# Optimization experiments

Hardware: AMD Instinct MI355X
Metric: run time of the kernel (lower is better)

## Reference

```python
import jax, jax.numpy as jnp
import numpy as np

B, C_IN, C_H, C_OUT, H, W = 2, 512, 512, 512, 14, 14


def setup_inputs() -> dict:
    key = jax.random.key(0)
    ks = jax.random.split(key, 6)
    s_in = 1.0 / np.sqrt(C_IN + C_H)   # torch Linear init bound for in_linear
    s_out = 1.0 / np.sqrt(C_H)          # torch Linear init bound for out_linear
    return {
        "input": jax.random.normal(ks[0], (B, C_IN, H, W), jnp.float32),
        # in_linear weight (C_H, C_IN + C_H) split into x-part and h-part
        "Wx": jax.random.uniform(ks[1], (C_H, C_IN), jnp.float32, -s_in, s_in),
        "Wh": jax.random.uniform(ks[2], (C_H, C_H), jnp.float32, -s_in, s_in),
        "b_in": jax.random.uniform(ks[3], (C_H,), jnp.float32, -s_in, s_in),
        "Wo": jax.random.uniform(ks[4], (C_OUT, C_H), jnp.float32, -s_out, s_out),
        "b_out": jax.random.uniform(ks[5], (C_OUT,), jnp.float32, -s_out, s_out),
    }


def reference(input, Wx, Wh, b_in, Wo, b_out):
    Bn, _, Hn, Wn = input.shape
    hid = Wh.shape[0]
    # four scan directions = four flips of the input (outputs are summed in
    # flipped coordinates, exactly as the original torch code does -- no unflip)
    x_modes = jnp.stack([
        input,
        jnp.flip(input, 3),
        jnp.flip(input, 2),
        jnp.flip(jnp.flip(input, 2), 3),
    ])  # (4, B, C_IN, H, W)
    rows = jnp.arange(Hn)
    cols = jnp.arange(Wn)

    def run_mode(x):
        # x-contribution of in_linear, shared by every (i,j) in the window
        a = jnp.einsum('hc,bcxy->bhxy', Wx, x) + b_in[None, :, None, None]

        def step(h, p):
            px, py = p // Wn, p % Wn
            # h_vivj over the full grid; cells outside the causal window hold
            # h == 0 and are masked out of the sum below (softmax is per-pixel
            # over channels, so no cross-pixel contamination)
            z = jax.nn.relu(a[:, :, px, py][:, :, None, None]
                            + jnp.einsum('ch,bhxy->bcxy', Wh, h))
            sm = jax.nn.softmax(z, axis=1)  # Softmax(dim=1): over channels
            mask = (rows[:, None] <= px) & (cols[None, :] <= py)  # (H, W)
            h_vi = jnp.sum(z * sm * mask, axis=(2, 3))  # (B, hid)
            h = h.at[:, :, px, py].set(h_vi)
            y_vi = h_vi @ Wo.T + b_out
            return h, y_vi

        h0 = jnp.zeros((Bn, hid, Hn, Wn), input.dtype)
        _, ys = jax.lax.scan(step, h0, jnp.arange(Hn * Wn))
        # ys: (H*W, B, C_OUT) -> (B, C_OUT, H, W) in raster order
        return ys.reshape(Hn, Wn, Bn, -1).transpose(2, 3, 0, 1)

    y = jax.vmap(run_mode)(x_modes).sum(axis=0)  # sum over the 4 directions
    return jax.nn.softmax(y, axis=1)
```

## Files before the change

kernel.cpp:

```cpp
#include <hip/hip_runtime.h>
#include <hip/hip_bf16.h>

#define BB 2
#define CC 512
#define HH 14
#define WW 14
#define PP 196
#define NSEQ 8
#define NSLICE 8
#define NWORK (14 * NSLICE)
#define FW 16
#define NZERO (3 * PP * FW)
#define ALL8 0x0101010101010101ull


__global__ __launch_bounds__(256) void prep(
    const float* __restrict__ Wx, const float* __restrict__ X,
    const float* __restrict__ b_in, const float* __restrict__ Wh,
    float* __restrict__ A, float* __restrict__ WhT,
    unsigned* __restrict__ cnts ) {
    __shared__ float Ws[32][33], Xs[32][33];
    int bid = blockIdx.x;
    int t = threadIdx.x;
    if (bid < 224) {
        int z = bid / 112, rem = bid % 112;
        int c0 = (rem % 16) * 32, p0 = (rem / 16) * 32;
        int tx = t % 32, ty = t / 32;
        int pl = (t % 16) * 2, cl = (t / 16) * 2;
        float acc[2][2] = {{0.f,0.f},{0.f,0.f}};
        for (int k0 = 0; k0 < CC; k0 += 32) {
            #pragma unroll
            for (int r = 0; r < 4; ++r)
                Ws[ty + 8*r][tx] = Wx[(size_t)(c0 + ty + 8*r) * CC + k0 + tx];
            #pragma unroll
            for (int r = 0; r < 4; ++r) {
                int p = p0 + tx, k = k0 + ty + 8*r;
                Xs[ty + 8*r][tx] = (p < PP) ? X[((size_t)z * CC + k) * PP + p] : 0.f;
            }
            __syncthreads();
            #pragma unroll
            for (int k = 0; k < 32; ++k) {
                float w0 = Ws[cl][k], w1 = Ws[cl+1][k];
                float x0 = Xs[k][pl], x1 = Xs[k][pl+1];
                acc[0][0] += w0*x0; acc[0][1] += w0*x1;
                acc[1][0] += w1*x0; acc[1][1] += w1*x1;
            }
            __syncthreads();
        }
        #pragma unroll
        for (int i = 0; i < 2; ++i)
            #pragma unroll
            for (int j = 0; j < 2; ++j) {
                int c = c0 + cl + i, p = p0 + pl + j;
                if (p < PP) A[((size_t)z * PP + p) * CC + c] = acc[i][j] + b_in[c];
            }
    } else if (bid < 480) {
        int tid = bid - 224;
        int c0 = (tid % 16) * 32, k0 = (tid / 16) * 32;
        int tx = t % 32, ty = t / 32;
        #pragma unroll
        for (int r = 0; r < 4; ++r)
            Ws[ty + 8*r][tx] = Wh[(size_t)(c0 + ty + 8*r) * CC + k0 + tx];
        __syncthreads();
        #pragma unroll
        for (int r = 0; r < 4; ++r)
            WhT[(size_t)(k0 + ty + 8*r) * CC + c0 + tx] = Ws[tx][ty + 8*r];
    } else {
        for (int i = t; i < NZERO; i += 256) cnts[i] = 0u;
    }
}

__device__ __forceinline__ unsigned long long flag8_ld(const unsigned char* f) {
    return __hip_atomic_load((const unsigned long long*)f, __ATOMIC_RELAXED,
                             __HIP_MEMORY_SCOPE_AGENT);
}
__device__ __forceinline__ void flag_st(unsigned char* f) {
    __hip_atomic_store(f, (unsigned char)1, __ATOMIC_RELAXED,
                       __HIP_MEMORY_SCOPE_AGENT);
}
__device__ __forceinline__ float ldf_agent(const float* p) {
    return __hip_atomic_load(p, __ATOMIC_RELAXED, __HIP_MEMORY_SCOPE_AGENT);
}
__device__ __forceinline__ void store_wt(float* p, float v) {
    __hip_atomic_store(p, v, __ATOMIC_RELAXED, __HIP_MEMORY_SCOPE_AGENT);
}

__device__ __forceinline__ void pix(const float4 E0, const float4 E1,
                                    const float* ar, const float* er, float* hacc) {
    float ee[8] = {E0.x,E0.y,E0.z,E0.w,E1.x,E1.y,E1.z,E1.w};
    float ds = 0.f, tl[8];
    #pragma unroll
    for (int j = 0; j < 8; ++j) {
        float sv = ar[j] + __logf(ee[j]);
        float pv = er[j] * ee[j];
        ds += fmaxf(pv, 1.0f);
        tl[j] = fmaxf(sv, 0.0f) * pv;
    }
    #pragma unroll
    for (int off = 32; off; off >>= 1) ds += __shfl_xor(ds, off, 64);
    float rd = 1.0f / ds;
    #pragma unroll
    for (int j = 0; j < 8; ++j) hacc[j] += tl[j] * rd;
}

__device__ __forceinline__ void proc_row(const float* __restrict__ rowp, int n,
                                         const float* ar, const float* er, float* hacc) {
    float4 cur[4][2];
    int y = 0, curn = (n < 4) ? n : 4;
    #pragma unroll
    for (int i = 0; i < 4; ++i) if (i < curn) {
        cur[i][0] = *(const float4*)(rowp + (size_t)i * CC);
        cur[i][1] = *(const float4*)(rowp + (size_t)i * CC + 256);
    }
    while (true) {
        int yn = y + curn;
        int rem = n - yn;
        int nextn = (rem < 4) ? rem : 4;
        float4 nxt[4][2];
        #pragma unroll
        for (int i = 0; i < 4; ++i) if (i < nextn) {
            nxt[i][0] = *(const float4*)(rowp + (size_t)(yn + i) * CC);
            nxt[i][1] = *(const float4*)(rowp + (size_t)(yn + i) * CC + 256);
        }
        #pragma unroll
        for (int i = 0; i < 4; ++i) if (i < curn)
            pix(cur[i][0], cur[i][1], ar, er, hacc);
        if (nextn <= 0) break;
        #pragma unroll
        for (int i = 0; i < 4; ++i) if (i < nextn) {
            cur[i][0] = nxt[i][0]; cur[i][1] = nxt[i][1];
        }
        curn = nextn; y = yn;
    }
}

__global__ __launch_bounds__(512, 2) void rnn_dataflow(
    const float* __restrict__ A, const float* __restrict__ WhT,
    float* __restrict__ E, float* __restrict__ h_bulk,
    float* __restrict__ h_t, float* __restrict__ TLN,
    float* __restrict__ TLW, float* __restrict__ dsAcc,
    unsigned char* __restrict__ uflag, unsigned char* __restrict__ hflag) {
    __shared__ __align__(16) float hT8[CC * 8];
    __shared__ __align__(16) float up[8 * 576];
    __shared__ unsigned mbox;
    __shared__ unsigned pf;
    int bid = blockIdx.x;
    int t = threadIdx.x;
    int lane = t & 63, wv = t >> 6;

    if (bid < NWORK) {
        int px = bid >> 3, w = bid & 7;
        int ch = w * 64 + lane;
        int m = wv >> 1, b = wv & 1;
        float wreg2[64];
        #pragma unroll
        for (int kk = 0; kk < 64; ++kk)
            wreg2[kk] = WhT[(size_t)(wv * 64 + kk) * CC + ch];
        __builtin_amdgcn_s_setprio(1);

        float hb[8];
        float tnr[8], dsNr[8];
        bool hb_ok = false;
        bool n_ok  = false;

        for (int py = 0; py < WW; ++py) {
            int cell = px * WW + py;
            int cellN = cell - WW, cellW = cell - 1;

            float aSr = 0.f, aWr = 0.f;
            if (px < HH - 1) {
                int fi = (m & 2) ? (HH - 2 - px) : (px + 1);
                int fj = (m & 1) ? (WW - 1 - py) : py;
                aSr = A[((size_t)b * PP + fi * WW + fj) * CC + ch];
            }
            if (py < WW - 1) {
                int fi = (m & 2) ? (HH - 1 - px) : px;
                int fj = (m & 1) ? (WW - 2 - py) : (py + 1);
                aWr = A[((size_t)b * PP + fi * WW + fj) * CC + ch];
            }

            if (!hb_ok) {
                if (wv == 0 && lane == 0)
                    while (flag8_ld(hflag + (size_t)cell * 64) != ALL8)
                        __builtin_amdgcn_s_sleep(1);
                __syncthreads();
                asm volatile("" ::: "memory");
                #pragma unroll
                for (int s = 0; s < 8; ++s)
                    hb[s] = h_bulk[((size_t)cell * NSEQ + s) * CC + t];
            }

            if (wv == 0) {
                while (true) {
                    unsigned ok = 1u;
                    if (lane == 0)      { if (py > 0) ok = (flag8_ld(uflag + (size_t)cellW * 64) == ALL8); }
                    else if (lane == 1) { if (px > 0 && !n_ok) ok = (flag8_ld(uflag + (size_t)cellN * 64) == ALL8); }
                    if (__ballot(ok != 0u) == ~0ull) break;
                    __builtin_amdgcn_s_sleep(1);
                }
            }
            __syncthreads();
            asm volatile("" ::: "memory");

            if (px > 0) {
                if (!n_ok) {
                    #pragma unroll
                    for (int i = 0; i < 8; ++i)
                        dsNr[i] = ldf_agent(&dsAcc[(size_t)cell * 16 + i]);
                    #pragma unroll
                    for (int s = 0; s < 8; ++s)
                        tnr[s] = ldf_agent(&TLN[((size_t)cell * NSEQ + s) * CC + t]);
                }
                #pragma unroll
                for (int s = 0; s < 8; ++s)
                    hb[s] += tnr[s] * __builtin_amdgcn_rcpf(dsNr[s]);
            }
            if (py > 0) {
                float dsw[8], tw[8];
                #pragma unroll
                for (int i = 0; i < 8; ++i)
                    dsw[i] = ldf_agent(&dsAcc[(size_t)cell * 16 + 8 + i]);
                #pragma unroll
                for (int s = 0; s < 8; ++s)
                    tw[s] = ldf_agent(&TLW[((size_t)cell * NSEQ + s) * CC + t]);
                #pragma unroll
                for (int s = 0; s < 8; ++s)
                    hb[s] += tw[s] * __builtin_amdgcn_rcpf(dsw[s]);
            }
            if (wv == w) {
                #pragma unroll
                for (int s = 0; s < 8; ++s)
                    h_t[((size_t)cell * NSEQ + s) * CC + t] = hb[s];
            }
            *(float4*)&hT8[t * 8]     = make_float4(hb[0], hb[1], hb[2], hb[3]);
            *(float4*)&hT8[t * 8 + 4] = make_float4(hb[4], hb[5], hb[6], hb[7]);
            if (cell == PP - 1) break;

            float acc[8] = {0.f,0.f,0.f,0.f,0.f,0.f,0.f,0.f};
            const float* hp = hT8 + (wv << 9);
            #pragma unroll
            for (int kk = 0; kk < 64; ++kk) {
                float4 h0 = *(const float4*)(hp + kk * 8);
                float4 h1 = *(const float4*)(hp + kk * 8 + 4);
                float wvv = wreg2[kk];
                acc[0] += wvv * h0.x; acc[1] += wvv * h0.y;
                acc[2] += wvv * h0.z; acc[3] += wvv * h0.w;
                acc[4] += wvv * h1.x; acc[5] += wvv * h1.y;
                acc[6] += wvv * h1.z; acc[7] += wvv * h1.w;
            }
            #pragma unroll
            for (int s = 0; s < 8; ++s)
                up[wv * 576 + lane * 9 + s] = acc[s];
            __syncthreads();

            {
                float U = up[lane * 9 + wv];
                #pragma unroll
                for (int w2 = 1; w2 < 8; ++w2) U += up[w2 * 576 + lane * 9 + wv];
                float Ev = __expf(U);
                store_wt(&E[((size_t)wv * PP + cell) * CC + ch], Ev);
                float pdS = 0.f, pdW = 0.f;
                if (px < HH - 1) {
                    float pv = __expf(aSr) * Ev;
                    store_wt(&TLN[((size_t)(cell + WW) * NSEQ + wv) * CC + ch],
                             fmaxf(aSr + U, 0.f) * pv);
                    pdS = fmaxf(pv, 1.f);
                }
                if (py < WW - 1) {
                    float pv = __expf(aWr) * Ev;
                    store_wt(&TLW[((size_t)(cell + 1) * NSEQ + wv) * CC + ch],
                             fmaxf(aWr + U, 0.f) * pv);
                    pdW = fmaxf(pv, 1.f);
                }
                #pragma unroll
                for (int off = 32; off; off >>= 1) {
                    pdS += __shfl_xor(pdS, off, 64);
                    pdW += __shfl_xor(pdW, off, 64);
                }
                if (lane == 0) {
                    if (px < HH - 1)
                        unsafeAtomicAdd(&dsAcc[(size_t)(cell + WW) * 16 + wv], pdS);
                    if (py < WW - 1)
                        unsafeAtomicAdd(&dsAcc[(size_t)(cell + 1) * 16 + 8 + wv], pdW);
                }
            }

            if (t == 0) {
                unsigned v = 0u;
                if (py + 1 < WW) {
                    if (flag8_ld(hflag + (size_t)(cell + 1) * 64) == ALL8) v |= 1u;
                    if (px > 0 &&
                        flag8_ld(uflag + (size_t)(cellN + 1) * 64) == ALL8) v |= 2u;
                }
                pf = v;
            }

            __syncthreads();
            if (t == 0) flag_st(uflag + (size_t)cell * 64 + w);

            hb_ok = false; n_ok = false;
            if (py + 1 < WW) {
                unsigned v = pf;
                if (v & 1u) {
                    #pragma unroll
                    for (int s = 0; s < 8; ++s)
                        hb[s] = h_bulk[((size_t)(cell + 1) * NSEQ + s) * CC + t];
                    hb_ok = true;
                }
                if (v & 2u) {
                    #pragma unroll
                    for (int i = 0; i < 8; ++i)
                        dsNr[i] = ldf_agent(&dsAcc[(size_t)(cell + 1) * 16 + i]);
                    #pragma unroll
                    for (int s = 0; s < 8; ++s)
                        tnr[s] = ldf_agent(&TLN[((size_t)(cell + 1) * NSEQ + s) * CC + t]);
                    n_ok = true;
                }
            }
        }
    } else {
        int cell = bid - NWORK;
        int px = cell / WW, py = cell % WW;
        int s = wv, m = s >> 1, b = s & 1;
        int fi = (m & 2) ? (HH-1-px) : px;
        int fj = (m & 1) ? (WW-1-py) : py;
        int cb = lane * 4;

        if (t == 0) mbox = 0u;
        __syncthreads();

        const float* acur = A + ((size_t)b * PP + fi * WW + fj) * CC;
        float4 a0 = *(const float4*)(acur + cb);
        float4 a1 = *(const float4*)(acur + cb + 256);
        float ar[8] = {a0.x,a0.y,a0.z,a0.w,a1.x,a1.y,a1.z,a1.w};
        float er[8];
        #pragma unroll
        for (int j = 0; j < 8; ++j) er[j] = __expf(ar[j]);
        float hacc[8] = {0.f,0.f,0.f,0.f,0.f,0.f,0.f,0.f};

        {
            float ds = 0.f, tl[8];
            #pragma unroll
            for (int j = 0; j < 8; ++j) {
                float pv = er[j];
                ds += fmaxf(pv, 1.0f);
                tl[j] = fmaxf(ar[j], 0.0f) * pv;
            }
            #pragma unroll
            for (int off = 32; off; off >>= 1) ds += __shfl_xor(ds, off, 64);
            float rd = 1.0f / ds;
            #pragma unroll
            for (int j = 0; j < 8; ++j) hacc[j] += tl[j] * rd;
        }

        const float* Eb = E + (size_t)s * PP * CC;
        int sx = lane >> 1, sph = lane & 1;
        int gate = -1;
        if (sx <= px) {
            int L = (sx <= px-2) ? py : ((sx == px-1) ? py-1 : py-2);
            if (L >= 0) {
                if (L <= 2) { if (sph == 0) gate = sx * WW + L; }
                else gate = sx * WW + (sph ? L : (L - 3));
            }
        }
        unsigned pend = (unsigned)__ballot(gate >= 0);

        if (wv == 0) {
            unsigned done = 0u;
            while (pend) {
                bool rdy = true;
                if (gate >= 0 && ((pend >> lane) & 1u))
                    rdy = (flag8_ld(uflag + (size_t)gate * 64) == ALL8);
                unsigned newly = pend & (unsigned)__ballot(rdy);
                if (!newly) { __builtin_amdgcn_s_sleep(2); continue; }
                done |= newly;
                __hip_atomic_store(&mbox, done, __ATOMIC_RELAXED,
                                   __HIP_MEMORY_SCOPE_WORKGROUP);
                asm volatile("" ::: "memory");
                unsigned go = newly;
                while (go) {
                    int sl = __ffs(go) - 1; go &= go - 1;
                    int xx = sl >> 1;
                    int L = (xx <= px-2) ? py : ((xx == px-1) ? py-1 : py-2);
                    int yy0 = 0, yy1 = L;
                    if (L > 2) { if (sl & 1) yy0 = L - 2; else yy1 = L - 3; }
                    proc_row(Eb + (size_t)(xx * WW + yy0) * CC + cb,
                             yy1 - yy0 + 1, ar, er, hacc);
                }
                pend &= ~newly;
            }
        } else {
            while (pend) {
                unsigned d = __hip_atomic_load(&mbox, __ATOMIC_RELAXED,
                                               __HIP_MEMORY_SCOPE_WORKGROUP);
                unsigned newly = d & pend;
                if (!newly) { __builtin_amdgcn_s_sleep(2); continue; }
                asm volatile("" ::: "memory");
                unsigned go = newly;
                while (go) {
                    int sl = __ffs(go) - 1; go &= go - 1;
                    int xx = sl >> 1;
                    int L = (xx <= px-2) ? py : ((xx == px-1) ? py-1 : py-2);
                    int yy0 = 0, yy1 = L;
                    if (L > 2) { if (sl & 1) yy0 = L - 2; else yy1 = L - 3; }
                    proc_row(Eb + (size_t)(xx * WW + yy0) * CC + cb,
                             yy1 - yy0 + 1, ar, er, hacc);
                }
                pend &= ~newly;
            }
        }

        float* hp = h_bulk + ((size_t)cell * NSEQ + s) * CC;
        #pragma unroll
        for (int j = 0; j < 4; ++j) {
            store_wt(hp + cb + j,       hacc[j]);
            store_wt(hp + cb + 256 + j, hacc[4 + j]);
        }
        __builtin_amdgcn_s_waitcnt(0);
        asm volatile("" ::: "memory");
        if (lane == 0) flag_st(hflag + (size_t)cell * 64 + s);
    }
}

__global__ __launch_bounds__(256) void gemm_y(
    const float* __restrict__ Wo, const float* __restrict__ h_t,
    const float* __restrict__ b_out, float* __restrict__ Y) {
    __shared__ float Ws[32][33], Hs[32][33];
    int b  = blockIdx.z;
    int c0 = blockIdx.x * 32, p0 = blockIdx.y * 32;
    int t  = threadIdx.x;
    int tx = t % 32, ty = t / 32;
    int pl = (t % 16) * 2, cl = (t / 16) * 2;
    float acc[2][2] = {{0.f,0.f},{0.f,0.f}};
    for (int k0 = 0; k0 < CC; k0 += 32) {
        #pragma unroll
        for (int r = 0; r < 4; ++r)
            Ws[ty + 8*r][tx] = Wo[(size_t)(c0 + ty + 8*r) * CC + k0 + tx];
        #pragma unroll
        for (int r = 0; r < 4; ++r) {
            int p = p0 + ty + 8*r;
            float v = 0.f;
            if (p < PP) {
                size_t base = (size_t)p * NSEQ * CC + k0 + tx;
                v = h_t[base + (size_t)(0 + b) * CC]
                  + h_t[base + (size_t)(2 + b) * CC]
                  + h_t[base + (size_t)(4 + b) * CC]
                  + h_t[base + (size_t)(6 + b) * CC];
            }
            Hs[tx][ty + 8*r] = v;
        }
        __syncthreads();
        #pragma unroll
        for (int k = 0; k < 32; ++k) {
            float w0 = Ws[cl][k], w1 = Ws[cl+1][k];
            float h0 = Hs[k][pl], h1 = Hs[k][pl+1];
            acc[0][0] += w0*h0; acc[0][1] += w0*h1;
            acc[1][0] += w1*h0; acc[1][1] += w1*h1;
        }
        __syncthreads();
    }
    #pragma unroll
    for (int i = 0; i < 2; ++i)
        #pragma unroll
        for (int j = 0; j < 2; ++j) {
            int cc = c0 + cl + i, p = p0 + pl + j;
            if (p < PP) Y[((size_t)b * PP + p) * CC + cc] = acc[i][j] + 4.0f * b_out[cc];
        }
}

__global__ __launch_bounds__(256) void softmax_out(
    const float* __restrict__ Y, float* __restrict__ out) {
    int wave = threadIdx.x >> 6, lane = threadIdx.x & 63;
    int idx = blockIdx.x * 4 + wave;
    if (idx >= BB * PP) return;
    int b = idx / PP, p = idx % PP;
    const float* y = Y + ((size_t)b * PP + p) * CC;
    float v[8];
    float mx = -3.4e38f;
    #pragma unroll
    for (int j = 0; j < 8; ++j) { v[j] = y[lane + 64*j]; mx = fmaxf(mx, v[j]); }
    #pragma unroll
    for (int off = 32; off; off >>= 1) mx = fmaxf(mx, __shfl_xor(mx, off, 64));
    float sum = 0.f;
    #pragma unroll
    for (int j = 0; j < 8; ++j) { v[j] = expf(v[j] - mx); sum += v[j]; }
    #pragma unroll
    for (int off = 32; off; off >>= 1) sum += __shfl_xor(sum, off, 64);
    float r = 1.0f / sum;
    #pragma unroll
    for (int j = 0; j < 8; ++j)
        out[((size_t)b * CC + lane + 64*j) * PP + p] = v[j] * r;
}

extern "C" void kernel_launch(void* const* d_in, const int* in_sizes, int n_in,
                              void* d_out, int out_size, void* d_ws, size_t ws_size,
                              hipStream_t stream) {
    const float* X     = (const float*)d_in[0];
    const float* Wx    = (const float*)d_in[1];
    const float* Wh    = (const float*)d_in[2];
    const float* b_in  = (const float*)d_in[3];
    const float* Wo    = (const float*)d_in[4];
    const float* b_out = (const float*)d_in[5];
    float* out = (float*)d_out;

    float* ws     = (float*)d_ws;
    float* WhT    = ws;
    float* A      = WhT    + 262144;
    float* E      = A      + 200704;
    float* h_bulk = E      + 802816;
    float* h_t    = h_bulk + 802816;
    float* TLN    = h_t    + 802816;
    float* TLW    = TLN    + 802816;
    float* Y      = TLW    + 802816;
    unsigned char* uflag = (unsigned char*)(Y + 200704);
    unsigned char* hflag = uflag + PP * 64;
    float* dsAcc = (float*)(hflag + PP * 64);

    hipLaunchKernelGGL(prep, dim3(481), dim3(256), 0, stream,
                       Wx, X, b_in, Wh, A, WhT, (unsigned*)uflag);
    hipLaunchKernelGGL(rnn_dataflow, dim3(NWORK + PP), dim3(512), 0, stream,
                       A, WhT, E, h_bulk, h_t, TLN, TLW, dsAcc, uflag, hflag);
    hipLaunchKernelGGL(gemm_y, dim3(16, 7, 2), dim3(256), 0, stream, Wo, h_t, b_out, Y);
    hipLaunchKernelGGL(softmax_out, dim3(98), dim3(256), 0, stream, Y, out);
}
```

Baseline: 349.9 us.

## Fuse output projection and softmax into dataflow kernel via per-cell flags

Measured after the change: 319.4 us. 1.1x faster.

```diff
diff --git a/kernel.cpp b/kernel.cpp
--- a/kernel.cpp
+++ b/kernel.cpp
@@ -17,7 +17,8 @@
 __global__ __launch_bounds__(256) void prep(
     const float* __restrict__ Wx, const float* __restrict__ X,
     const float* __restrict__ b_in, const float* __restrict__ Wh,
-    float* __restrict__ A, float* __restrict__ WhT,
+    const float* __restrict__ Wo,
+    float* __restrict__ A, float* __restrict__ WhT, float* __restrict__ WoT,
     unsigned* __restrict__ cnts ) {
     __shared__ float Ws[32][33], Xs[32][33];
     int bid = blockIdx.x;
@@ -54,17 +55,20 @@
                 int c = c0 + cl + i, p = p0 + pl + j;
                 if (p < PP) A[((size_t)z * PP + p) * CC + c] = acc[i][j] + b_in[c];
             }
-    } else if (bid < 480) {
+    } else if (bid < 736) {
         int tid = bid - 224;
+        const float* src = (tid < 256) ? Wh : Wo;
+        float* dst = (tid < 256) ? WhT : WoT;
+        tid &= 255;
         int c0 = (tid % 16) * 32, k0 = (tid / 16) * 32;
         int tx = t % 32, ty = t / 32;
         #pragma unroll
         for (int r = 0; r < 4; ++r)
-            Ws[ty + 8*r][tx] = Wh[(size_t)(c0 + ty + 8*r) * CC + k0 + tx];
+            Ws[ty + 8*r][tx] = src[(size_t)(c0 + ty + 8*r) * CC + k0 + tx];
         __syncthreads();
         #pragma unroll
         for (int r = 0; r < 4; ++r)
-            WhT[(size_t)(k0 + ty + 8*r) * CC + c0 + tx] = Ws[tx][ty + 8*r];
+            dst[(size_t)(k0 + ty + 8*r) * CC + c0 + tx] = Ws[tx][ty + 8*r];
     } else {
         for (int i = t; i < NZERO; i += 256) cnts[i] = 0u;
     }
@@ -139,7 +143,9 @@
     float* __restrict__ E, float* __restrict__ h_bulk,
     float* __restrict__ h_t, float* __restrict__ TLN,
     float* __restrict__ TLW, float* __restrict__ dsAcc,
-    unsigned char* __restrict__ uflag, unsigned char* __restrict__ hflag) {
+    unsigned char* __restrict__ uflag, unsigned char* __restrict__ hflag,
+    const float* __restrict__ WoT, const float* __restrict__ b_out,
+    float* __restrict__ out) {
     __shared__ __align__(16) float hT8[CC * 8];
     __shared__ __align__(16) float up[8 * 576];
     __shared__ unsigned mbox;
@@ -230,11 +236,17 @@
             if (wv == w) {
                 #pragma unroll
                 for (int s = 0; s < 8; ++s)
-                    h_t[((size_t)cell * NSEQ + s) * CC + t] = hb[s];
+                    store_wt(&h_t[((size_t)cell * NSEQ + s) * CC + t], hb[s]);
             }
             *(float4*)&hT8[t * 8]     = make_float4(hb[0], hb[1], hb[2], hb[3]);
             *(float4*)&hT8[t * 8 + 4] = make_float4(hb[4], hb[5], hb[6], hb[7]);
-            if (cell == PP - 1) break;
+            if (cell == PP - 1) {
+                __builtin_amdgcn_s_waitcnt(0);
+                asm volatile("" ::: "memory");
+                if (wv == w && lane == 0)
+                    flag_st(uflag + (size_t)cell * 64 + w);
+                break;
+            }
 
             float acc[8] = {0.f,0.f,0.f,0.f,0.f,0.f,0.f,0.f};
             const float* hp = hT8 + (wv << 9);
@@ -318,7 +330,7 @@
                 }
             }
         }
-    } else {
+    } else if (bid < NWORK + PP) {
         int cell = bid - NWORK;
         int px = cell / WW, py = cell % WW;
         int s = wv, m = s >> 1, b = s & 1;
@@ -419,77 +431,70 @@
         __builtin_amdgcn_s_waitcnt(0);
         asm volatile("" ::: "memory");
         if (lane == 0) flag_st(hflag + (size_t)cell * 64 + s);
+    } else {
+        int p = bid - NWORK - PP;
+        float2* hs2 = (float2*)hT8;
+        float (*redm)[2] = (float (*)[2])up;
+        float (*reds)[2] = (float (*)[2])(up + 64);
+
+        if (t == 0)
+            while (flag8_ld(uflag + (size_t)p * 64) != ALL8)
+                __builtin_amdgcn_s_sleep(8);
+        __syncthreads();
+        asm volatile("" ::: "memory");
+
+        {
+            float v[8];
+            #pragma unroll
+            for (int s = 0; s < 8; ++s)
+                v[s] = ldf_agent(&h_t[((size_t)p * NSEQ + s) * CC + t]);
+            hs2[t] = make_float2(v[0]+v[2]+v[4]+v[6], v[1]+v[3]+v[5]+v[7]);
+        }
+        __syncthreads();
+
+        float y0 = 4.0f * b_out[t], y1 = y0;
+        for (int k0 = 0; k0 < CC; k0 += 8) {
+            float wk[8];
+            #pragma unroll
+            for (int j = 0; j < 8; ++j)
+                wk[j] = WoT[(size_t)(k0 + j) * CC + t];
+            #pragma unroll
+            for (int j = 0; j < 8; ++j) {
+                float2 hk = hs2[k0 + j];
+                y0 += wk[j] * hk.x;
+                y1 += wk[j] * hk.y;
+            }
+        }
+
+        float m0 = y0, m1 = y1;
+        #pragma unroll
+        for (int off = 32; off; off >>= 1) {
+            m0 = fmaxf(m0, __shfl_xor(m0, off, 64));
+            m1 = fmaxf(m1, __shfl_xor(m1, off, 64));
+        }
+        if (lane == 0) { redm[wv][0] = m0; redm[wv][1] = m1; }
+        __syncthreads();
+        float gm0 = redm[0][0], gm1 = redm[0][1];
+        #pragma unroll
+        for (int i = 1; i < 8; ++i) {
+            gm0 = fmaxf(gm0, redm[i][0]);
+            gm1 = fmaxf(gm1, redm[i][1]);
+        }
+        float e0 = expf(y0 - gm0), e1 = expf(y1 - gm1);
+        float s0 = e0, s1 = e1;
+        #pragma unroll
+        for (int off = 32; off; off >>= 1) {
+            s0 += __shfl_xor(s0, off, 64);
+            s1 += __shfl_xor(s1, off, 64);
+        }
+        if (lane == 0) { reds[wv][0] = s0; reds[wv][1] = s1; }
+        __syncthreads();
+        float t0 = 0.f, t1 = 0.f;
+        #pragma unroll
+        for (int i = 0; i < 8; ++i) { t0 += reds[i][0]; t1 += reds[i][1]; }
+        out[((size_t)0 * CC + t) * PP + p] = e0 * (1.0f / t0);
+        out[((size_t)1 * CC + t) * PP + p] = e1 * (1.0f / t1);
     }
-}
-
-__global__ __launch_bounds__(256) void gemm_y(
-    const float* __restrict__ Wo, const float* __restrict__ h_t,
-    const float* __restrict__ b_out, float* __restrict__ Y) {
-    __shared__ float Ws[32][33], Hs[32][33];
-    int b  = blockIdx.z;
-    int c0 = blockIdx.x * 32, p0 = blockIdx.y * 32;
-    int t  = threadIdx.x;
-    int tx = t % 32, ty = t / 32;
-    int pl = (t % 16) * 2, cl = (t / 16) * 2;
-    float acc[2][2] = {{0.f,0.f},{0.f,0.f}};
-    for (int k0 = 0; k0 < CC; k0 += 32) {
-        #pragma unroll
-        for (int r = 0; r < 4; ++r)
-            Ws[ty + 8*r][tx] = Wo[(size_t)(c0 + ty + 8*r) * CC + k0 + tx];
-        #pragma unroll
-        for (int r = 0; r < 4; ++r) {
-            int p = p0 + ty + 8*r;
-            float v = 0.f;
-            if (p < PP) {
-                size_t base = (size_t)p * NSEQ * CC + k0 + tx;
-                v = h_t[base + (size_t)(0 + b) * CC]
-                  + h_t[base + (size_t)(2 + b) * CC]
-                  + h_t[base + (size_t)(4 + b) * CC]
-                  + h_t[base + (size_t)(6 + b) * CC];
-            }
-            Hs[tx][ty + 8*r] = v;
-        }
-        __syncthreads();
-        #pragma unroll
-        for (int k = 0; k < 32; ++k) {
-            float w0 = Ws[cl][k], w1 = Ws[cl+1][k];
-            float h0 = Hs[k][pl], h1 = Hs[k][pl+1];
-            acc[0][0] += w0*h0; acc[0][1] += w0*h1;
-            acc[1][0] += w1*h0; acc[1][1] += w1*h1;
-        }
-        __syncthreads();
-    }
-    #pragma unroll
-    for (int i = 0; i < 2; ++i)
-        #pragma unroll
-        for (int j = 0; j < 2; ++j) {
-            int cc = c0 + cl + i, p = p0 + pl + j;
-            if (p < PP) Y[((size_t)b * PP + p) * CC + cc] = acc[i][j] + 4.0f * b_out[cc];
-        }
-}
-
-__global__ __launch_bounds__(256) void softmax_out(
-    const float* __restrict__ Y, float* __restrict__ out) {
-    int wave = threadIdx.x >> 6, lane = threadIdx.x & 63;
-    int idx = blockIdx.x * 4 + wave;
-    if (idx >= BB * PP) return;
-    int b = idx / PP, p = idx % PP;
-    const float* y = Y + ((size_t)b * PP + p) * CC;
-    float v[8];
-    float mx = -3.4e38f;
-    #pragma unroll
-    for (int j = 0; j < 8; ++j) { v[j] = y[lane + 64*j]; mx = fmaxf(mx, v[j]); }
-    #pragma unroll
-    for (int off = 32; off; off >>= 1) mx = fmaxf(mx, __shfl_xor(mx, off, 64));
-    float sum = 0.f;
-    #pragma unroll
-    for (int j = 0; j < 8; ++j) { v[j] = expf(v[j] - mx); sum += v[j]; }
-    #pragma unroll
-    for (int off = 32; off; off >>= 1) sum += __shfl_xor(sum, off, 64);
-    float r = 1.0f / sum;
-    #pragma unroll
-    for (int j = 0; j < 8; ++j)
-        out[((size_t)b * CC + lane + 64*j) * PP + p] = v[j] * r;
 }
 
 extern "C" void kernel_launch(void* const* d_in, const int* in_sizes, int n_in,
@@ -511,15 +516,14 @@
     float* h_t    = h_bulk + 802816;
     float* TLN    = h_t    + 802816;
     float* TLW    = TLN    + 802816;
-    float* Y      = TLW    + 802816;
-    unsigned char* uflag = (unsigned char*)(Y + 200704);
+    float* WoT    = TLW    + 802816;
+    unsigned char* uflag = (unsigned char*)(WoT + 262144);
     unsigned char* hflag = uflag + PP * 64;
     float* dsAcc = (float*)(hflag + PP * 64);
 
-    hipLaunchKernelGGL(prep, dim3(481), dim3(256), 0, stream,
-                       Wx, X, b_in, Wh, A, WhT, (unsigned*)uflag);
-    hipLaunchKernelGGL(rnn_dataflow, dim3(NWORK + PP), dim3(512), 0, stream,
-                       A, WhT, E, h_bulk, h_t, TLN, TLW, dsAcc, uflag, hflag);
-    hipLaunchKernelGGL(gemm_y, dim3(16, 7, 2), dim3(256), 0, stream, Wo, h_t, b_out, Y);
-    hipLaunchKernelGGL(softmax_out, dim3(98), dim3(256), 0, stream, Y, out);
-}
+    hipLaunchKernelGGL(prep, dim3(737), dim3(256), 0, stream,
+                       Wx, X, b_in, Wh, Wo, A, WhT, WoT, (unsigned*)uflag);
+    hipLaunchKernelGGL(rnn_dataflow, dim3(NWORK + PP + PP), dim3(512), 0, stream,
+                       A, WhT, E, h_bulk, h_t, TLN, TLW, dsAcc, uflag, hflag,
+                       WoT, b_out, out);
+}
```
